# Kernel optimization log

Measured on AMD Instinct MI355X. Metric: run time of the kernel, lower is better.

Reference implementation:

```python
import jax, jax.numpy as jnp
import numpy as np


def _seg_mean(h_src, src, dst, n_dst):
    # gather neighbor features along edges, then segment-mean onto dst nodes
    msgs = h_src[src]                                  # [E, F]
    s = jax.ops.segment_sum(msgs, dst, num_segments=n_dst)
    deg = jax.ops.segment_sum(jnp.ones_like(dst, dtype=h_src.dtype), dst, num_segments=n_dst)
    return s / jnp.maximum(deg, 1.0)[:, None]          # zero-degree -> 0


def _sage_conv(h_src, h_dst, src, dst, n_dst, W, b):
    h_N = _seg_mean(h_src, src, dst, n_dst)            # [n_dst, F]
    h_total = jnp.concatenate([h_dst, h_N], axis=1)    # [n_dst, 2F]
    return h_total @ W + b


def setup_inputs() -> dict:
    key = jax.random.key(0)
    ks = jax.random.split(key, 10)
    n_src1, n_dst1, n_dst2 = 200000, 50000, 10000
    E1, E2 = 1000000, 200000
    in_f, h_f, n_cls = 256, 256, 64
    x = jax.random.normal(ks[0], (n_src1, in_f), dtype=jnp.float32)
    W1 = jax.random.normal(ks[1], (2 * in_f, h_f), dtype=jnp.float32) * (1.0 / np.sqrt(2 * in_f))
    b1 = jax.random.normal(ks[2], (h_f,), dtype=jnp.float32) * 0.01
    W2 = jax.random.normal(ks[3], (2 * h_f, n_cls), dtype=jnp.float32) * (1.0 / np.sqrt(2 * h_f))
    b2 = jax.random.normal(ks[4], (n_cls,), dtype=jnp.float32) * 0.01
    src1 = jax.random.randint(ks[5], (E1,), 0, n_src1, dtype=jnp.int32)
    dst1 = jax.random.randint(ks[6], (E1,), 0, n_dst1, dtype=jnp.int32)
    src2 = jax.random.randint(ks[7], (E2,), 0, n_dst1, dtype=jnp.int32)
    dst2 = jax.random.randint(ks[8], (E2,), 0, n_dst2, dtype=jnp.int32)
    return {"x": x, "W1": W1, "b1": b1, "W2": W2, "b2": b2,
            "src1": src1, "dst1": dst1, "src2": src2, "dst2": dst2,
            "n_dst1": n_dst1, "n_dst2": n_dst2}


def reference(x, W1, b1, W2, b2, src1, dst1, src2, dst2, n_dst1, n_dst2):
    h_dst = x[:n_dst1]
    h = _sage_conv(x, h_dst, src1, dst1, n_dst1, W1, b1)
    h = jax.nn.relu(h)
    h_dst2 = h[:n_dst2]
    out = _sage_conv(h, h_dst2, src2, dst2, n_dst2, W2, b2)
    return out
```

## Files before the change

kernel.cpp:

```cpp
#include <hip/hip_runtime.h>
#include <hip/hip_bf16.h>

#define N_DST1 50000
#define N_DST2 10000
#define FEAT   256

typedef unsigned int u32;
typedef __attribute__((ext_vector_type(4))) float f32x4;
typedef __attribute__((ext_vector_type(8))) short bf16x8;

__device__ __forceinline__ ushort f2bf(float f) {
    u32 u = __float_as_uint(f);
    u32 r = (u + 0x7FFFu + ((u >> 16) & 1u)) >> 16;
    return (ushort)r;
}
__device__ __forceinline__ float bf2f(ushort u) {
    return __uint_as_float(((u32)u) << 16);
}

__device__ __forceinline__ void gload_lds16(const void* g, void* l) {
    __builtin_amdgcn_global_load_lds(
        (const __attribute__((address_space(1))) u32*)g,
        (__attribute__((address_space(3))) u32*)l, 16, 0, 0);
}

__global__ void count_deg2_kernel(const int* __restrict__ dst1, int E1, int* __restrict__ deg1,
                                  const int* __restrict__ dst2, int E2, int* __restrict__ deg2) {
    int i = blockIdx.x * blockDim.x + threadIdx.x;
    if (i < E1) atomicAdd(&deg1[dst1[i]], 1);
    else {
        int k = i - E1;
        if (k < E2) atomicAdd(&deg2[dst2[k]], 1);
    }
}

__global__ void scatter_csr2_kernel(const int* __restrict__ src1, const int* __restrict__ dst1,
                                    int E1, int* __restrict__ pos1, int* __restrict__ csr1,
                                    const int* __restrict__ src2, const int* __restrict__ dst2,
                                    int E2, int* __restrict__ pos2, int* __restrict__ csr2) {
    int i = blockIdx.x * blockDim.x + threadIdx.x;
    if (i < E1) {
        int slot = atomicAdd(&pos1[dst1[i]], 1);
        csr1[slot] = src1[i];
    } else {
        int k = i - E1;
        if (k < E2) {
            int slot = atomicAdd(&pos2[dst2[k]], 1);
            csr2[slot] = src2[k];
        }
    }
}

__global__ void excl_scan2_kernel(const int* __restrict__ degA, int nA, int* __restrict__ offA, int* __restrict__ posA,
                                  const int* __restrict__ degB, int nB, int* __restrict__ offB, int* __restrict__ posB) {
    const int* deg = (blockIdx.x == 0) ? degA : degB;
    int*       off = (blockIdx.x == 0) ? offA : offB;
    int*       pos = (blockIdx.x == 0) ? posA : posB;
    int n = (blockIdx.x == 0) ? nA : nB;
    int n4 = n >> 2;

    __shared__ int wsum[16];
    __shared__ int carry_s;
    int t = threadIdx.x;
    int lane = t & 63, wid = t >> 6;
    if (t == 0) carry_s = 0;
    __syncthreads();
    for (int base = 0; base < n4; base += 1024) {
        int i = base + t;
        int4 v = make_int4(0, 0, 0, 0);
        if (i < n4) v = reinterpret_cast<const int4*>(deg)[i];
        int tot = v.x + v.y + v.z + v.w;
        int s = tot;
        #pragma unroll
        for (int d = 1; d < 64; d <<= 1) {
            int u = __shfl_up(s, d, 64);
            if (lane >= d) s += u;
        }
        if (lane == 63) wsum[wid] = s;
        __syncthreads();
        if (wid == 0 && lane < 16) {
            int ws = wsum[lane];
            #pragma unroll
            for (int d = 1; d < 16; d <<= 1) {
                int u = __shfl_up(ws, d, 64);
                if (lane >= d) ws += u;
            }
            wsum[lane] = ws;
        }
        __syncthreads();
        int waveoff = (wid == 0) ? 0 : wsum[wid - 1];
        int carry = carry_s;
        int base0 = carry + waveoff + s - tot;
        if (i < n4) {
            int4 e;
            e.x = base0;
            e.y = base0 + v.x;
            e.z = base0 + v.x + v.y;
            e.w = base0 + v.x + v.y + v.z;
            reinterpret_cast<int4*>(off)[i] = e;
            reinterpret_cast<int4*>(pos)[i] = e;
        }
        __syncthreads();
        if (t == 0) carry_s = carry + wsum[15];
        __syncthreads();
    }
    if (t == 0) off[n] = carry_s;
}

__global__ void cvt_bf16_kernel(const float* __restrict__ in, ushort* __restrict__ out, int n8) {
    int i = blockIdx.x * blockDim.x + threadIdx.x;
    if (i >= n8) return;
    const float4* p = (const float4*)in + (size_t)i * 2;
    float4 a = p[0], b = p[1];
    ushort4 lo = make_ushort4(f2bf(a.x), f2bf(a.y), f2bf(a.z), f2bf(a.w));
    ushort4 hi = make_ushort4(f2bf(b.x), f2bf(b.y), f2bf(b.z), f2bf(b.w));
    ushort4* q = (ushort4*)out + (size_t)i * 2;
    q[0] = lo; q[1] = hi;
}

__global__ void cvt_wt2_kernel(const float* __restrict__ W1, ushort* __restrict__ W1T,
                               const float* __restrict__ W2, ushort* __restrict__ W2T) {
    int k = blockIdx.x;
    int t = threadIdx.x;
    if (t < 256) W1T[(size_t)t * 512 + k] = f2bf(W1[(size_t)k * 256 + t]);
    else {
        int n = t - 256;
        W2T[(size_t)n * 512 + k] = f2bf(W2[(size_t)k * 64 + n]);
    }
}

__global__ void seg_mean_bf16_kernel(const ushort* __restrict__ X, const int* __restrict__ off,
                                     const int* __restrict__ csr, ushort* __restrict__ out) {
    int d = blockIdx.x;
    int l = threadIdx.x;
    int half = l >> 5;
    int f8 = (l & 31) * 8;
    int beg = off[d], end = off[d + 1];
    float acc[8] = {0.f, 0.f, 0.f, 0.f, 0.f, 0.f, 0.f, 0.f};
    int j = beg;
    for (; j + 8 <= end; j += 8) {
        #pragma unroll
        for (int p = 0; p < 4; ++p) {
            int r = csr[j + p * 2 + half];
            bf16x8 v = *reinterpret_cast<const bf16x8*>(&X[(size_t)r * FEAT + f8]);
            #pragma unroll
            for (int q = 0; q < 8; ++q) acc[q] += bf2f((ushort)v[q]);
        }
    }
    for (; j < end; j += 2) {
        int idx = j + half;
        float m = (idx < end) ? 1.f : 0.f;
        int r = csr[min(idx, end - 1)];
        bf16x8 v = *reinterpret_cast<const bf16x8*>(&X[(size_t)r * FEAT + f8]);
        #pragma unroll
        for (int q = 0; q < 8; ++q) acc[q] += m * bf2f((ushort)v[q]);
    }
    #pragma unroll
    for (int q = 0; q < 8; ++q) acc[q] += __shfl_xor(acc[q], 32);
    if (l < 32) {
        float sc = 1.0f / (float)max(end - beg, 1);
        bf16x8 ov;
        #pragma unroll
        for (int q = 0; q < 8; ++q) ov[q] = (short)f2bf(acc[q] * sc);
        *reinterpret_cast<bf16x8*>(&out[(size_t)d * FEAT + f8]) = ov;
    }
}

__global__ void seg_mean_f32_kernel(const float* __restrict__ X, const int* __restrict__ off,
                                    const int* __restrict__ csr, ushort* __restrict__ out) {
    int d = blockIdx.x;
    int t = threadIdx.x;
    int beg = off[d], end = off[d + 1];
    float a0 = 0.f, a1 = 0.f, a2 = 0.f, a3 = 0.f;
    for (int j = beg; j < end; ++j) {
        int s = csr[j];
        float4 v = *reinterpret_cast<const float4*>(&X[(size_t)s * FEAT + t * 4]);
        a0 += v.x; a1 += v.y; a2 += v.z; a3 += v.w;
    }
    float sc = 1.0f / (float)max(end - beg, 1);
    ushort4 o = make_ushort4(f2bf(a0 * sc), f2bf(a1 * sc), f2bf(a2 * sc), f2bf(a3 * sc));
    *reinterpret_cast<ushort4*>(&out[(size_t)d * FEAT + t * 4]) = o;
}

template<int BM, int BN, int WGM, int WGN, bool RELU, bool OBF16>
__global__ __launch_bounds__(WGM * WGN * 64)
void gemm_mfma_kernel(const ushort* __restrict__ A0, const ushort* __restrict__ A1,
                      const ushort* __restrict__ BT, const float* __restrict__ bias,
                      ushort* __restrict__ Cb, float* __restrict__ Cf,
                      int M, int Nfull) {
    constexpr int NWAVE = WGM * WGN;
    constexpr int WM = BM / WGM;
    constexpr int WN = BN / WGN;
    constexpr int MF = WM / 16;
    constexpr int NF = WN / 16;
    constexpr int ACH = BM / 16;
    constexpr int BCH = BN / 16;

    __shared__ ushort Al[2][BM][32];
    __shared__ ushort Bl[2][BN][32];

    const int t = threadIdx.x;
    const int lane = t & 63;
    const int wid = t >> 6;
    const int wm = wid / WGN, wn = wid % WGN;
    const int lr = lane & 15, grp = lane >> 4;
    const int rowBase = blockIdx.y * BM;
    const int colBase = blockIdx.x * BN;

    f32x4 acc[MF][NF];
    #pragma unroll
    for (int m = 0; m < MF; ++m)
        #pragma unroll
        for (int n = 0; n < NF; ++n)
            acc[m][n] = (f32x4){0.f, 0.f, 0.f, 0.f};

    auto stage = [&](int buf, int kt) {
        const ushort* Asrc = (kt < 8) ? A0 : A1;
        const int kcol = (kt * 32) & 255;
        #pragma unroll
        for (int ch = wid; ch < ACH; ch += NWAVE) {
            int r = ch * 16 + (lane >> 2);
            int rg = min(rowBase + r, M - 1);
            int c = lane & 3;
            int ksw = (c ^ (r & 3)) * 8;
            gload_lds16(&Asrc[(size_t)rg * 256 + kcol + ksw], &Al[buf][ch * 16][0]);
        }
        #pragma unroll
        for (int ch = wid; ch < BCH; ch += NWAVE) {
            int r = ch * 16 + (lane >> 2);
            int c = lane & 3;
            int ksw = (c ^ (r & 3)) * 8;
            gload_lds16(&BT[(size_t)(colBase + r) * 512 + kt * 32 + ksw], &Bl[buf][ch * 16][0]);
        }
    };

    stage(0, 0);
    __syncthreads();

    int buf = 0;
    for (int kt = 0; kt < 16; ++kt) {
        if (kt + 1 < 16) stage(buf ^ 1, kt + 1);
        bf16x8 af[MF], bfr[NF];
        #pragma unroll
        for (int m = 0; m < MF; ++m) {
            int r = wm * WM + m * 16 + lr;
            af[m] = *reinterpret_cast<const bf16x8*>(
                (const char*)&Al[buf][0][0] + r * 64 + ((grp ^ (r & 3)) << 4));
        }
        #pragma unroll
        for (int n = 0; n < NF; ++n) {
            int r = wn * WN + n * 16 + lr;
            bfr[n] = *reinterpret_cast<const bf16x8*>(
                (const char*)&Bl[buf][0][0] + r * 64 + ((grp ^ (r & 3)) << 4));
        }
        #pragma unroll
        for (int m = 0; m < MF; ++m)
            #pragma unroll
            for (int n = 0; n < NF; ++n)
                acc[m][n] = __builtin_amdgcn_mfma_f32_16x16x32_bf16(af[m], bfr[n], acc[m][n], 0, 0, 0);
        __syncthreads();
        buf ^= 1;
    }

    #pragma unroll
    for (int m = 0; m < MF; ++m) {
        #pragma unroll
        for (int q = 0; q < 4; ++q) {
            int rowg = rowBase + wm * WM + m * 16 + grp * 4 + q;
            if (rowg >= M) continue;
            #pragma unroll
            for (int n = 0; n < NF; ++n) {
                int colg = colBase + wn * WN + n * 16 + lr;
                float v = acc[m][n][q] + bias[colg];
                if (RELU) v = fmaxf(v, 0.f);
                if (OBF16) Cb[(size_t)rowg * Nfull + colg] = f2bf(v);
                else       Cf[(size_t)rowg * Nfull + colg] = v;
            }
        }
    }
}

extern "C" void kernel_launch(void* const* d_in, const int* in_sizes, int n_in,
                              void* d_out, int out_size, void* d_ws, size_t ws_size,
                              hipStream_t stream) {
    const float* x  = (const float*)d_in[0];
    const float* W1 = (const float*)d_in[1];
    const float* b1 = (const float*)d_in[2];
    const float* W2 = (const float*)d_in[3];
    const float* b2 = (const float*)d_in[4];
    const int* src1 = (const int*)d_in[5];
    const int* dst1 = (const int*)d_in[6];
    const int* src2 = (const int*)d_in[7];
    const int* dst2 = (const int*)d_in[8];
    const int E1 = in_sizes[5];
    const int E2 = in_sizes[7];
    const int N_SRC1 = in_sizes[0] / FEAT;
    float* out = (float*)d_out;

    char* ws = (char*)d_ws;
    size_t o = 0;
    auto carve = [&](size_t bytes) { char* p = ws + o; o = (o + bytes + 255) & ~(size_t)255; return p; };
    int*    degs = (int*)   carve((size_t)(N_DST1 + N_DST2) * 4);
    int*    deg1 = degs;
    int*    deg2 = degs + N_DST1;
    int*    off1 = (int*)   carve((size_t)(N_DST1 + 1) * 4);
    int*    pos1 = (int*)   carve((size_t)N_DST1 * 4);
    int*    csr1 = (int*)   carve((size_t)E1 * 4);
    ushort* hN1b = (ushort*)carve((size_t)N_DST1 * FEAT * 2);
    ushort* hb   = (ushort*)carve((size_t)N_DST1 * FEAT * 2);
    int*    off2 = (int*)   carve((size_t)(N_DST2 + 1) * 4);
    int*    pos2 = (int*)   carve((size_t)N_DST2 * 4);
    int*    csr2 = (int*)   carve((size_t)E2 * 4);
    ushort* hN2b = (ushort*)carve((size_t)N_DST2 * FEAT * 2);
    ushort* W1T  = (ushort*)carve((size_t)256 * 512 * 2);
    ushort* W2T  = (ushort*)carve((size_t)64 * 512 * 2);
    size_t full_bytes = (size_t)N_SRC1 * FEAT * 2;
    bool full = (o + full_bytes) <= ws_size;
    ushort* xb = (ushort*)carve(full ? full_bytes : (size_t)N_DST1 * FEAT * 2);

    hipMemsetAsync(degs, 0, (size_t)(N_DST1 + N_DST2) * 4, stream);
    {
        int tot = E1 + E2;
        count_deg2_kernel<<<(tot + 255) / 256, 256, 0, stream>>>(dst1, E1, deg1, dst2, E2, deg2);
        excl_scan2_kernel<<<2, 1024, 0, stream>>>(deg1, N_DST1, off1, pos1, deg2, N_DST2, off2, pos2);
        scatter_csr2_kernel<<<(tot + 255) / 256, 256, 0, stream>>>(
            src1, dst1, E1, pos1, csr1, src2, dst2, E2, pos2, csr2);
    }

    {
        int n8 = (full ? N_SRC1 : N_DST1) * FEAT / 8;
        cvt_bf16_kernel<<<(n8 + 255) / 256, 256, 0, stream>>>(x, xb, n8);
    }
    cvt_wt2_kernel<<<512, 320, 0, stream>>>(W1, W1T, W2, W2T);

    if (full)
        seg_mean_bf16_kernel<<<N_DST1, 64, 0, stream>>>(xb, off1, csr1, hN1b);
    else
        seg_mean_f32_kernel<<<N_DST1, 64, 0, stream>>>(x, off1, csr1, hN1b);
    gemm_mfma_kernel<128, 256, 2, 4, true, true><<<dim3(1, (N_DST1 + 127) / 128), 512, 0, stream>>>(
        xb, hN1b, W1T, b1, hb, nullptr, N_DST1, 256);

    seg_mean_bf16_kernel<<<N_DST2, 64, 0, stream>>>(hb, off2, csr2, hN2b);
    gemm_mfma_kernel<64, 64, 2, 2, false, false><<<dim3(1, (N_DST2 + 63) / 64), 256, 0, stream>>>(
        hb, hN2b, W2T, b2, nullptr, out, N_DST2, 64);
}
```

Before: 337.2 us.

## Fuse preprocessing kernels and pack multiple segments per block in seg-mean

Merges the bf16 conversion of x with degree counting into one prep kernel that uses nontemporal loads, and merges the exclusive scan with the weight transpose/convert into one launch. This cuts the number of kernel launches in the preprocessing chain. The segment-mean kernel now processes 8 destination nodes per 512-thread block instead of one node per 64-thread block, and uses a single masked 8-wide loop in place of the separate tail loop. In exchange, partial tail chunks now issue redundant masked loads, and the scan blocks share a launch with 512 mostly idle 1024-thread weight blocks.

```diff
diff --git a/kernel.cpp b/kernel.cpp
--- a/kernel.cpp
+++ b/kernel.cpp
@@ -24,14 +24,98 @@
         (__attribute__((address_space(3))) u32*)l, 16, 0, 0);
 }
 
-__global__ void count_deg2_kernel(const int* __restrict__ dst1, int E1, int* __restrict__ deg1,
-                                  const int* __restrict__ dst2, int E2, int* __restrict__ deg2) {
-    int i = blockIdx.x * blockDim.x + threadIdx.x;
-    if (i < E1) atomicAdd(&deg1[dst1[i]], 1);
-    else {
-        int k = i - E1;
-        if (k < E2) atomicAdd(&deg2[dst2[k]], 1);
-    }
+__global__ __launch_bounds__(256) void prep_kernel(
+    const float* __restrict__ x, ushort* __restrict__ xb, int n8,
+    const int* __restrict__ dst1, int E1, int* __restrict__ deg1,
+    const int* __restrict__ dst2, int E2, int* __restrict__ deg2)
+{
+    int gid = blockIdx.x * blockDim.x + threadIdx.x;
+    if (gid < n8) {
+        const f32x4* p = (const f32x4*)x + (size_t)gid * 2;
+        f32x4 a = __builtin_nontemporal_load(p);
+        f32x4 b = __builtin_nontemporal_load(p + 1);
+        ushort4 lo = make_ushort4(f2bf(a.x), f2bf(a.y), f2bf(a.z), f2bf(a.w));
+        ushort4 hi = make_ushort4(f2bf(b.x), f2bf(b.y), f2bf(b.z), f2bf(b.w));
+        ushort4* q = (ushort4*)xb + (size_t)gid * 2;
+        q[0] = lo; q[1] = hi;
+    } else {
+        int e = gid - n8;
+        if (e < E1) atomicAdd(&deg1[dst1[e]], 1);
+        else {
+            int k = e - E1;
+            if (k < E2) atomicAdd(&deg2[dst2[k]], 1);
+        }
+    }
+}
+
+__global__ __launch_bounds__(1024) void scan_wt_kernel(
+    const int* __restrict__ degA, int nA, int* __restrict__ offA, int* __restrict__ posA,
+    const int* __restrict__ degB, int nB, int* __restrict__ offB, int* __restrict__ posB,
+    const float* __restrict__ W1, ushort* __restrict__ W1T,
+    const float* __restrict__ W2, ushort* __restrict__ W2T)
+{
+    if (blockIdx.x >= 2) {
+        int k = blockIdx.x - 2;
+        int t = threadIdx.x;
+        if (t < 256) W1T[(size_t)t * 512 + k] = f2bf(W1[(size_t)k * 256 + t]);
+        else if (t < 320) {
+            int n = t - 256;
+            W2T[(size_t)n * 512 + k] = f2bf(W2[(size_t)k * 64 + n]);
+        }
+        return;
+    }
+    const int* deg = (blockIdx.x == 0) ? degA : degB;
+    int*       off = (blockIdx.x == 0) ? offA : offB;
+    int*       pos = (blockIdx.x == 0) ? posA : posB;
+    int n = (blockIdx.x == 0) ? nA : nB;
+    int n4 = n >> 2;
+
+    __shared__ int wsum[16];
+    __shared__ int carry_s;
+    int t = threadIdx.x;
+    int lane = t & 63, wid = t >> 6;
+    if (t == 0) carry_s = 0;
+    __syncthreads();
+    for (int base = 0; base < n4; base += 1024) {
+        int i = base + t;
+        int4 v = make_int4(0, 0, 0, 0);
+        if (i < n4) v = reinterpret_cast<const int4*>(deg)[i];
+        int tot = v.x + v.y + v.z + v.w;
+        int s = tot;
+        #pragma unroll
+        for (int d = 1; d < 64; d <<= 1) {
+            int u = __shfl_up(s, d, 64);
+            if (lane >= d) s += u;
+        }
+        if (lane == 63) wsum[wid] = s;
+        __syncthreads();
+        if (wid == 0 && lane < 16) {
+            int ws = wsum[lane];
+            #pragma unroll
+            for (int d = 1; d < 16; d <<= 1) {
+                int u = __shfl_up(ws, d, 64);
+                if (lane >= d) ws += u;
+            }
+            wsum[lane] = ws;
+        }
+        __syncthreads();
+        int waveoff = (wid == 0) ? 0 : wsum[wid - 1];
+        int carry = carry_s;
+        int base0 = carry + waveoff + s - tot;
+        if (i < n4) {
+            int4 e;
+            e.x = base0;
+            e.y = base0 + v.x;
+            e.z = base0 + v.x + v.y;
+            e.w = base0 + v.x + v.y + v.z;
+            reinterpret_cast<int4*>(off)[i] = e;
+            reinterpret_cast<int4*>(pos)[i] = e;
+        }
+        __syncthreads();
+        if (t == 0) carry_s = carry + wsum[15];
+        __syncthreads();
+    }
+    if (t == 0) off[n] = carry_s;
 }
 
 __global__ void scatter_csr2_kernel(const int* __restrict__ src1, const int* __restrict__ dst1,
@@ -51,109 +135,28 @@
     }
 }
 
-__global__ void excl_scan2_kernel(const int* __restrict__ degA, int nA, int* __restrict__ offA, int* __restrict__ posA,
-                                  const int* __restrict__ degB, int nB, int* __restrict__ offB, int* __restrict__ posB) {
-    const int* deg = (blockIdx.x == 0) ? degA : degB;
-    int*       off = (blockIdx.x == 0) ? offA : offB;
-    int*       pos = (blockIdx.x == 0) ? posA : posB;
-    int n = (blockIdx.x == 0) ? nA : nB;
-    int n4 = n >> 2;
-
-    __shared__ int wsum[16];
-    __shared__ int carry_s;
-    int t = threadIdx.x;
-    int lane = t & 63, wid = t >> 6;
-    if (t == 0) carry_s = 0;
-    __syncthreads();
-    for (int base = 0; base < n4; base += 1024) {
-        int i = base + t;
-        int4 v = make_int4(0, 0, 0, 0);
-        if (i < n4) v = reinterpret_cast<const int4*>(deg)[i];
-        int tot = v.x + v.y + v.z + v.w;
-        int s = tot;
-        #pragma unroll
-        for (int d = 1; d < 64; d <<= 1) {
-            int u = __shfl_up(s, d, 64);
-            if (lane >= d) s += u;
-        }
-        if (lane == 63) wsum[wid] = s;
-        __syncthreads();
-        if (wid == 0 && lane < 16) {
-            int ws = wsum[lane];
-            #pragma unroll
-            for (int d = 1; d < 16; d <<= 1) {
-                int u = __shfl_up(ws, d, 64);
-                if (lane >= d) ws += u;
-            }
-            wsum[lane] = ws;
-        }
-        __syncthreads();
-        int waveoff = (wid == 0) ? 0 : wsum[wid - 1];
-        int carry = carry_s;
-        int base0 = carry + waveoff + s - tot;
-        if (i < n4) {
-            int4 e;
-            e.x = base0;
-            e.y = base0 + v.x;
-            e.z = base0 + v.x + v.y;
-            e.w = base0 + v.x + v.y + v.z;
-            reinterpret_cast<int4*>(off)[i] = e;
-            reinterpret_cast<int4*>(pos)[i] = e;
-        }
-        __syncthreads();
-        if (t == 0) carry_s = carry + wsum[15];
-        __syncthreads();
-    }
-    if (t == 0) off[n] = carry_s;
-}
-
-__global__ void cvt_bf16_kernel(const float* __restrict__ in, ushort* __restrict__ out, int n8) {
-    int i = blockIdx.x * blockDim.x + threadIdx.x;
-    if (i >= n8) return;
-    const float4* p = (const float4*)in + (size_t)i * 2;
-    float4 a = p[0], b = p[1];
-    ushort4 lo = make_ushort4(f2bf(a.x), f2bf(a.y), f2bf(a.z), f2bf(a.w));
-    ushort4 hi = make_ushort4(f2bf(b.x), f2bf(b.y), f2bf(b.z), f2bf(b.w));
-    ushort4* q = (ushort4*)out + (size_t)i * 2;
-    q[0] = lo; q[1] = hi;
-}
-
-__global__ void cvt_wt2_kernel(const float* __restrict__ W1, ushort* __restrict__ W1T,
-                               const float* __restrict__ W2, ushort* __restrict__ W2T) {
-    int k = blockIdx.x;
-    int t = threadIdx.x;
-    if (t < 256) W1T[(size_t)t * 512 + k] = f2bf(W1[(size_t)k * 256 + t]);
-    else {
-        int n = t - 256;
-        W2T[(size_t)n * 512 + k] = f2bf(W2[(size_t)k * 64 + n]);
-    }
-}
-
-__global__ void seg_mean_bf16_kernel(const ushort* __restrict__ X, const int* __restrict__ off,
-                                     const int* __restrict__ csr, ushort* __restrict__ out) {
-    int d = blockIdx.x;
-    int l = threadIdx.x;
+__global__ __launch_bounds__(512) void seg_mean_bf16_kernel(
+    const ushort* __restrict__ X, const int* __restrict__ off,
+    const int* __restrict__ csr, ushort* __restrict__ out, int ndst)
+{
+    int wid = threadIdx.x >> 6;
+    int d = blockIdx.x * 8 + wid;
+    if (d >= ndst) return;
+    int l = threadIdx.x & 63;
     int half = l >> 5;
     int f8 = (l & 31) * 8;
     int beg = off[d], end = off[d + 1];
     float acc[8] = {0.f, 0.f, 0.f, 0.f, 0.f, 0.f, 0.f, 0.f};
-    int j = beg;
-    for (; j + 8 <= end; j += 8) {
+    for (int j = beg; j < end; j += 8) {
         #pragma unroll
         for (int p = 0; p < 4; ++p) {
-            int r = csr[j + p * 2 + half];
+            int idx = j + p * 2 + half;
+            int r = csr[min(idx, end - 1)];
             bf16x8 v = *reinterpret_cast<const bf16x8*>(&X[(size_t)r * FEAT + f8]);
+            float m = (idx < end) ? 1.f : 0.f;
             #pragma unroll
-            for (int q = 0; q < 8; ++q) acc[q] += bf2f((ushort)v[q]);
-        }
-    }
-    for (; j < end; j += 2) {
-        int idx = j + half;
-        float m = (idx < end) ? 1.f : 0.f;
-        int r = csr[min(idx, end - 1)];
-        bf16x8 v = *reinterpret_cast<const bf16x8*>(&X[(size_t)r * FEAT + f8]);
-        #pragma unroll
-        for (int q = 0; q < 8; ++q) acc[q] += m * bf2f((ushort)v[q]);
+            for (int q = 0; q < 8; ++q) acc[q] += m * bf2f((ushort)v[q]);
+        }
     }
     #pragma unroll
     for (int q = 0; q < 8; ++q) acc[q] += __shfl_xor(acc[q], 32);
@@ -318,29 +321,27 @@
     bool full = (o + full_bytes) <= ws_size;
     ushort* xb = (ushort*)carve(full ? full_bytes : (size_t)N_DST1 * FEAT * 2);
 
-    hipMemsetAsync(degs, 0, (size_t)(N_DST1 + N_DST2) * 4, stream);
-    {
-        int tot = E1 + E2;
-        count_deg2_kernel<<<(tot + 255) / 256, 256, 0, stream>>>(dst1, E1, deg1, dst2, E2, deg2);
-        excl_scan2_kernel<<<2, 1024, 0, stream>>>(deg1, N_DST1, off1, pos1, deg2, N_DST2, off2, pos2);
-        scatter_csr2_kernel<<<(tot + 255) / 256, 256, 0, stream>>>(
-            src1, dst1, E1, pos1, csr1, src2, dst2, E2, pos2, csr2);
-    }
-
+    (void)hipMemsetAsync(degs, 0, (size_t)(N_DST1 + N_DST2) * 4, stream);
     {
         int n8 = (full ? N_SRC1 : N_DST1) * FEAT / 8;
-        cvt_bf16_kernel<<<(n8 + 255) / 256, 256, 0, stream>>>(x, xb, n8);
-    }
-    cvt_wt2_kernel<<<512, 320, 0, stream>>>(W1, W1T, W2, W2T);
+        int tot = n8 + E1 + E2;
+        prep_kernel<<<(tot + 255) / 256, 256, 0, stream>>>(
+            x, xb, n8, dst1, E1, deg1, dst2, E2, deg2);
+    }
+    scan_wt_kernel<<<514, 1024, 0, stream>>>(deg1, N_DST1, off1, pos1,
+                                             deg2, N_DST2, off2, pos2,
+                                             W1, W1T, W2, W2T);
+    scatter_csr2_kernel<<<(E1 + E2 + 255) / 256, 256, 0, stream>>>(
+        src1, dst1, E1, pos1, csr1, src2, dst2, E2, pos2, csr2);
 
     if (full)
-        seg_mean_bf16_kernel<<<N_DST1, 64, 0, stream>>>(xb, off1, csr1, hN1b);
+        seg_mean_bf16_kernel<<<(N_DST1 + 7) / 8, 512, 0, stream>>>(xb, off1, csr1, hN1b, N_DST1);
     else
         seg_mean_f32_kernel<<<N_DST1, 64, 0, stream>>>(x, off1, csr1, hN1b);
     gemm_mfma_kernel<128, 256, 2, 4, true, true><<<dim3(1, (N_DST1 + 127) / 128), 512, 0, stream>>>(
         xb, hN1b, W1T, b1, hb, nullptr, N_DST1, 256);
 
-    seg_mean_bf16_kernel<<<N_DST2, 64, 0, stream>>>(hb, off2, csr2, hN2b);
+    seg_mean_bf16_kernel<<<(N_DST2 + 7) / 8, 512, 0, stream>>>(hb, off2, csr2, hN2b, N_DST2);
     gemm_mfma_kernel<64, 64, 2, 2, false, false><<<dim3(1, (N_DST2 + 63) / 64), 256, 0, stream>>>(
         hb, hN2b, W2T, b2, nullptr, out, N_DST2, 64);
 }
```

After: 337.6 us. About the same (+0.1%).
